# Kernel optimization log

Measured on AMD Instinct MI355X. Metric: run time of the kernel, lower is better.

The kernel has to match this reference:

```python
import jax, jax.numpy as jnp
import numpy as np

TEMPERATURE = 0.5
EPS = 1e-8  # torch CosineSimilarity eps
NEG_INF = -1e9


def setup_inputs() -> dict:
    key = jax.random.key(0)
    k1, k2 = jax.random.split(key)
    B, D = 4096, 256
    return {
        "z_i": jax.random.normal(k1, (B, D), dtype=jnp.float32),
        "z_j": jax.random.normal(k2, (B, D), dtype=jnp.float32),
    }


def reference(z_i, z_j):
    B = z_i.shape[0]
    N = 2 * B
    z = jnp.concatenate([z_i, z_j], axis=0)  # [N, D]
    # Cosine similarity = GEMM of L2-normalized rows (same math as broadcasted CosineSimilarity)
    zn = z / jnp.maximum(jnp.linalg.norm(z, axis=1, keepdims=True), EPS)
    sim = (zn @ zn.T) / TEMPERATURE  # [N, N]
    # Positives: the (i, i+B) and (i+B, i) off-diagonals
    pos = jnp.concatenate([jnp.diagonal(sim, B), jnp.diagonal(sim, -B)])  # [N]
    # CE with label 0 over logits = [positive, negatives...]. The logit set per row
    # equals the sim row minus its self-diagonal entry (positive appears exactly once).
    sim_masked = jnp.where(jnp.eye(N, dtype=bool), NEG_INF, sim)
    lse = jax.nn.logsumexp(sim_masked, axis=1)  # [N]
    # CrossEntropyLoss(reduction='sum') / N == mean over rows
    return jnp.mean(lse - pos)
```

## Files before the change

kernel.cpp:

```cpp
#include <hip/hip_runtime.h>
#include <hip/hip_bf16.h>

#define NN 8192
#define BB 4096
#define DD 256
#define TILE 128
#define NT 64
#define NBLK 2080
#define KSCALE 2.8853900817779268f

typedef __attribute__((ext_vector_type(8))) short short8;
typedef __attribute__((ext_vector_type(4))) float f32x4;

static __device__ __forceinline__ float exp2_fast(float x) {
    float r; asm("v_exp_f32 %0, %1" : "=v"(r) : "v"(x)); return r;
}
static __device__ __forceinline__ ushort f2bf(float x) {
    __hip_bfloat16 h = __float2bfloat16(x);
    return *reinterpret_cast<ushort*>(&h);
}
static __device__ __forceinline__ float bf2f(short u) {
    unsigned int x = (unsigned int)(ushort)u << 16;
    float f; __builtin_memcpy(&f, &x, 4); return f;
}

__global__ __launch_bounds__(256) void norm_kernel(const float* __restrict__ zi,
                                                   const float* __restrict__ zj,
                                                   ushort* __restrict__ zn,
                                                   ushort* __restrict__ zns,
                                                   float* __restrict__ out) {
    if (blockIdx.x == 0 && threadIdx.x == 0) out[0] = 0.f;
    int row  = (blockIdx.x * 256 + threadIdx.x) >> 6;
    int lane = threadIdx.x & 63;
    const float* src = (row < BB) ? (zi + (size_t)row * DD)
                                  : (zj + (size_t)(row - BB) * DD);
    float4 v = ((const float4*)src)[lane];
    float ss = v.x * v.x + v.y * v.y + v.z * v.z + v.w * v.w;
    #pragma unroll
    for (int m = 32; m; m >>= 1) ss += __shfl_xor(ss, m, 64);
    float inv = 1.0f / fmaxf(sqrtf(ss), 1e-8f);
    ushort4 o, os;
    o.x  = f2bf(v.x * inv);            o.y  = f2bf(v.y * inv);
    o.z  = f2bf(v.z * inv);            o.w  = f2bf(v.w * inv);
    float invs = inv * KSCALE;
    os.x = f2bf(v.x * invs);           os.y = f2bf(v.y * invs);
    os.z = f2bf(v.z * invs);           os.w = f2bf(v.w * invs);
    ((ushort4*)(zn  + (size_t)row * DD))[lane] = o;
    ((ushort4*)(zns + (size_t)row * DD))[lane] = os;
}

__global__ __launch_bounds__(256) void sim_kernel(const ushort* __restrict__ zn,
                                                  const ushort* __restrict__ zns,
                                                  float* __restrict__ psum) {
    __shared__ int4  ldsA[2][512];
    __shared__ int4  ldsB[2][512];
    __shared__ float rsumL[2][2][64];
    __shared__ float csumL[2][2][64];

    const int tid  = threadIdx.x;
    const int w    = tid >> 6;
    const int lane = tid & 63;
    const int l15  = lane & 15;
    const int lhi  = lane >> 4;
    const int wr   = w >> 1;
    const int wc   = w & 1;

    int bid = blockIdx.x;
    int idx = (bid & 7) * (NBLK / 8) + (bid >> 3);
    int bj  = (int)((sqrtf(8.0f * (float)idx + 1.0f) - 1.0f) * 0.5f);
    while ((bj + 1) * (bj + 2) / 2 <= idx) ++bj;
    while (bj * (bj + 1) / 2 > idx) --bj;
    int bi = idx - bj * (bj + 1) / 2;

    const int  rowt0   = bi * TILE;
    const int  colt0   = bj * TILE;
    const bool offdiag = (bi != bj);

    auto STAGE = [&](int buf, int k) {
        #pragma unroll
        for (int i = 0; i < 2; ++i) {
            int d = i * 256 + tid;
            int r = d >> 2, g = d & 3;
            const ushort* sa = zns + (size_t)(rowt0 + r) * DD + k * 32 + g * 8;
            __builtin_amdgcn_global_load_lds(
                (__attribute__((address_space(1))) void*)sa,
                (__attribute__((address_space(3))) void*)&ldsA[buf][i * 256 + w * 64],
                16, 0, 0);
            const ushort* sb = zn + (size_t)(colt0 + r) * DD + k * 32 + g * 8;
            __builtin_amdgcn_global_load_lds(
                (__attribute__((address_space(1))) void*)sb,
                (__attribute__((address_space(3))) void*)&ldsB[buf][i * 256 + w * 64],
                16, 0, 0);
        }
    };

    f32x4 acc[4][4];
    #pragma unroll
    for (int mi = 0; mi < 4; ++mi)
        #pragma unroll
        for (int ni = 0; ni < 4; ++ni) acc[mi][ni] = (f32x4){0.f, 0.f, 0.f, 0.f};

    STAGE(0, 0);
    __syncthreads();

    #pragma unroll
    for (int k = 0; k < 8; ++k) {
        if (k < 7) STAGE((k + 1) & 1, k + 1);
        const short8* bufA = (const short8*)ldsA[k & 1];
        const short8* bufB = (const short8*)ldsB[k & 1];
        short8 af[4], bfr[4];
        #pragma unroll
        for (int mi = 0; mi < 4; ++mi)
            af[mi] = bufA[(wr * 64 + mi * 16 + l15) * 4 + lhi];
        #pragma unroll
        for (int ni = 0; ni < 4; ++ni)
            bfr[ni] = bufB[(wc * 64 + ni * 16 + l15) * 4 + lhi];
        #pragma unroll
        for (int mi = 0; mi < 4; ++mi)
            #pragma unroll
            for (int ni = 0; ni < 4; ++ni)
                acc[mi][ni] = __builtin_amdgcn_mfma_f32_16x16x32_bf16(af[mi], bfr[ni], acc[mi][ni], 0, 0, 0);
        __syncthreads();
    }

    float rpart[4][4];
    float cpart[4];
    #pragma unroll
    for (int mi = 0; mi < 4; ++mi)
        #pragma unroll
        for (int g = 0; g < 4; ++g) rpart[mi][g] = 0.f;
    #pragma unroll
    for (int ni = 0; ni < 4; ++ni) cpart[ni] = 0.f;

    #pragma unroll
    for (int mi = 0; mi < 4; ++mi)
        #pragma unroll
        for (int ni = 0; ni < 4; ++ni)
            #pragma unroll
            for (int g = 0; g < 4; ++g) {
                float e = exp2_fast(acc[mi][ni][g]);
                rpart[mi][g] += e;
                cpart[ni]    += e;
            }

    #pragma unroll
    for (int mi = 0; mi < 4; ++mi)
        #pragma unroll
        for (int g = 0; g < 4; ++g) {
            float v = rpart[mi][g];
            v += __shfl_xor(v, 1, 64); v += __shfl_xor(v, 2, 64);
            v += __shfl_xor(v, 4, 64); v += __shfl_xor(v, 8, 64);
            if (l15 == 0) rsumL[wr][wc][mi * 16 + lhi * 4 + g] = v;
        }
    #pragma unroll
    for (int ni = 0; ni < 4; ++ni) {
        float v = cpart[ni];
        v += __shfl_xor(v, 16, 64); v += __shfl_xor(v, 32, 64);
        if (lhi == 0) csumL[wc][wr][ni * 16 + l15] = v;
    }
    __syncthreads();

    if (tid < TILE)
        psum[(size_t)bj * NN + rowt0 + tid] =
            rsumL[tid >> 6][0][tid & 63] + rsumL[tid >> 6][1][tid & 63];
    if (offdiag && tid < TILE)
        psum[(size_t)bi * NN + colt0 + tid] =
            csumL[tid >> 6][0][tid & 63] + csumL[tid >> 6][1][tid & 63];
}

__global__ __launch_bounds__(1024) void reduce_kernel(const ushort* __restrict__ zn,
                                                      const ushort* __restrict__ zns,
                                                      const float* __restrict__ psum,
                                                      float* __restrict__ out) {
    const int tid  = threadIdx.x;
    const int rloc = tid >> 4;
    const int r    = blockIdx.x * 64 + rloc;
    const int l    = tid & 15;

    float S = 0.f;
    #pragma unroll
    for (int i = 0; i < 4; ++i) S += psum[(size_t)(i * 16 + l) * NN + r];

    const ushort* zr = zn  + (size_t)r * DD + l * 16;
    const ushort* sr = zns + (size_t)r * DD + l * 16;
    const ushort* pr = zn  + (size_t)(r ^ BB) * DD + l * 16;
    short8 z0 = *(const short8*)zr, z1 = *(const short8*)(zr + 8);
    short8 s0 = *(const short8*)sr, s1 = *(const short8*)(sr + 8);
    short8 p0 = *(const short8*)pr, p1 = *(const short8*)(pr + 8);
    float ds = 0.f, dp = 0.f;
    #pragma unroll
    for (int k = 0; k < 8; ++k) {
        float za = bf2f(z0[k]), zb = bf2f(z1[k]);
        ds += bf2f(s0[k]) * za + bf2f(s1[k]) * zb;
        dp += bf2f(p0[k]) * za + bf2f(p1[k]) * zb;
    }
    #pragma unroll
    for (int m = 1; m < 16; m <<= 1) {
        S  += __shfl_xor(S,  m, 64);
        ds += __shfl_xor(ds, m, 64);
        dp += __shfl_xor(dp, m, 64);
    }
    __shared__ float red[64];
    if (l == 0) red[rloc] = logf(S - exp2_fast(ds)) - 2.0f * dp;
    __syncthreads();
    if (tid < 64) {
        float v = red[tid];
        #pragma unroll
        for (int m = 32; m; m >>= 1) v += __shfl_xor(v, m, 64);
        if (tid == 0) atomicAdd(out, v * (1.0f / NN));
    }
}

extern "C" void kernel_launch(void* const* d_in, const int* in_sizes, int n_in,
                              void* d_out, int out_size, void* d_ws, size_t ws_size,
                              hipStream_t stream) {
    const float* zi = (const float*)d_in[0];
    const float* zj = (const float*)d_in[1];
    float* out = (float*)d_out;

    char* ws = (char*)d_ws;
    ushort* zn   = (ushort*)ws;
    ushort* zns  = (ushort*)(ws + (size_t)NN * DD * 2);
    float*  psum = (float*)(ws + (size_t)NN * DD * 4);

    norm_kernel<<<NN / 4, 256, 0, stream>>>(zi, zj, zn, zns, out);
    sim_kernel<<<NBLK, 256, 0, stream>>>(zn, zns, psum);
    reduce_kernel<<<NN / 64, 1024, 0, stream>>>(zn, zns, psum, out);
}
```

Baseline: 112.5 us.

## Enlarge sim tiles to 256 with 8 waves, swizzled LDS, and fine-grained waits

```diff
diff --git a/kernel.cpp b/kernel.cpp
--- a/kernel.cpp
+++ b/kernel.cpp
@@ -4,9 +4,10 @@
 #define NN 8192
 #define BB 4096
 #define DD 256
-#define TILE 128
-#define NT 64
-#define NBLK 2080
+#define TILE 256
+#define NT 32
+#define NBLK 528
+#define BK 32
 #define KSCALE 2.8853900817779268f
 
 typedef __attribute__((ext_vector_type(8))) short short8;
@@ -49,21 +50,22 @@
     ((ushort4*)(zns + (size_t)row * DD))[lane] = os;
 }
 
-__global__ __launch_bounds__(256) void sim_kernel(const ushort* __restrict__ zn,
-                                                  const ushort* __restrict__ zns,
-                                                  float* __restrict__ psum) {
-    __shared__ int4  ldsA[2][512];
-    __shared__ int4  ldsB[2][512];
-    __shared__ float rsumL[2][2][64];
-    __shared__ float csumL[2][2][64];
+__global__ __launch_bounds__(512)
+__attribute__((amdgpu_waves_per_eu(2, 2)))
+void sim_kernel(const ushort* __restrict__ zn,
+                const ushort* __restrict__ zns,
+                float* __restrict__ psum) {
+    __shared__ int4  lds4[2][2048];
+    __shared__ float rsum[2][4][128];
+    __shared__ float csum[4][2][64];
 
     const int tid  = threadIdx.x;
     const int w    = tid >> 6;
     const int lane = tid & 63;
     const int l15  = lane & 15;
     const int lhi  = lane >> 4;
-    const int wr   = w >> 1;
-    const int wc   = w & 1;
+    const int wr   = w >> 2;
+    const int wc   = w & 3;
 
     int bid = blockIdx.x;
     int idx = (bid & 7) * (NBLK / 8) + (bid >> 3);
@@ -78,62 +80,70 @@
 
     auto STAGE = [&](int buf, int k) {
         #pragma unroll
-        for (int i = 0; i < 2; ++i) {
-            int d = i * 256 + tid;
-            int r = d >> 2, g = d & 3;
-            const ushort* sa = zns + (size_t)(rowt0 + r) * DD + k * 32 + g * 8;
+        for (int i = 0; i < 4; ++i) {
+            int d = i * 512 + tid;
+            int s = d & 1023;
+            int r = s >> 2, gd = s & 3;
+            int gs = gd ^ ((r >> 2) & 3);
+            const ushort* srcp = (i < 2)
+                ? zns + (size_t)(rowt0 + r) * DD + k * BK + gs * 8
+                : zn  + (size_t)(colt0 + r) * DD + k * BK + gs * 8;
             __builtin_amdgcn_global_load_lds(
-                (__attribute__((address_space(1))) void*)sa,
-                (__attribute__((address_space(3))) void*)&ldsA[buf][i * 256 + w * 64],
+                (__attribute__((address_space(1))) void*)srcp,
+                (__attribute__((address_space(3))) void*)&lds4[buf][i * 512 + w * 64],
                 16, 0, 0);
-            const ushort* sb = zn + (size_t)(colt0 + r) * DD + k * 32 + g * 8;
-            __builtin_amdgcn_global_load_lds(
-                (__attribute__((address_space(1))) void*)sb,
-                (__attribute__((address_space(3))) void*)&ldsB[buf][i * 256 + w * 64],
-                16, 0, 0);
         }
     };
 
-    f32x4 acc[4][4];
-    #pragma unroll
-    for (int mi = 0; mi < 4; ++mi)
+    f32x4 acc[8][4];
+    #pragma unroll
+    for (int mi = 0; mi < 8; ++mi)
         #pragma unroll
         for (int ni = 0; ni < 4; ++ni) acc[mi][ni] = (f32x4){0.f, 0.f, 0.f, 0.f};
 
     STAGE(0, 0);
-    __syncthreads();
+    __builtin_amdgcn_sched_barrier(0);
 
     #pragma unroll
     for (int k = 0; k < 8; ++k) {
         if (k < 7) STAGE((k + 1) & 1, k + 1);
-        const short8* bufA = (const short8*)ldsA[k & 1];
-        const short8* bufB = (const short8*)ldsB[k & 1];
-        short8 af[4], bfr[4];
-        #pragma unroll
-        for (int mi = 0; mi < 4; ++mi)
-            af[mi] = bufA[(wr * 64 + mi * 16 + l15) * 4 + lhi];
-        #pragma unroll
-        for (int ni = 0; ni < 4; ++ni)
-            bfr[ni] = bufB[(wc * 64 + ni * 16 + l15) * 4 + lhi];
-        #pragma unroll
-        for (int mi = 0; mi < 4; ++mi)
+        __builtin_amdgcn_sched_barrier(0);
+        if (k < 7) asm volatile("s_waitcnt vmcnt(4)" ::: "memory");
+        else       asm volatile("s_waitcnt vmcnt(0)" ::: "memory");
+        __builtin_amdgcn_s_barrier();
+        __builtin_amdgcn_sched_barrier(0);
+
+        const short8* bufA = (const short8*)&lds4[k & 1][0];
+        const short8* bufB = (const short8*)&lds4[k & 1][1024];
+        short8 af[8], bf[4];
+        #pragma unroll
+        for (int mi = 0; mi < 8; ++mi) {
+            int r = wr * 128 + mi * 16 + l15;
+            af[mi] = bufA[r * 4 + (lhi ^ ((r >> 2) & 3))];
+        }
+        #pragma unroll
+        for (int ni = 0; ni < 4; ++ni) {
+            int r = wc * 64 + ni * 16 + l15;
+            bf[ni] = bufB[r * 4 + (lhi ^ ((r >> 2) & 3))];
+        }
+        #pragma unroll
+        for (int mi = 0; mi < 8; ++mi)
             #pragma unroll
             for (int ni = 0; ni < 4; ++ni)
-                acc[mi][ni] = __builtin_amdgcn_mfma_f32_16x16x32_bf16(af[mi], bfr[ni], acc[mi][ni], 0, 0, 0);
-        __syncthreads();
-    }
-
-    float rpart[4][4];
+                acc[mi][ni] = __builtin_amdgcn_mfma_f32_16x16x32_bf16(af[mi], bf[ni], acc[mi][ni], 0, 0, 0);
+    }
+
+    float rpart[8][4];
     float cpart[4];
     #pragma unroll
-    for (int mi = 0; mi < 4; ++mi)
+    for (int mi = 0; mi < 8; ++mi)
         #pragma unroll
         for (int g = 0; g < 4; ++g) rpart[mi][g] = 0.f;
     #pragma unroll
     for (int ni = 0; ni < 4; ++ni) cpart[ni] = 0.f;
 
     #pragma unroll
-    for (int mi = 0; mi < 4; ++mi)
+    for (int mi = 0; mi < 8; ++mi)
         #pragma unroll
         for (int ni = 0; ni < 4; ++ni)
             #pragma unroll
@@ -144,28 +154,31 @@
             }
 
     #pragma unroll
-    for (int mi = 0; mi < 4; ++mi)
+    for (int mi = 0; mi < 8; ++mi)
         #pragma unroll
         for (int g = 0; g < 4; ++g) {
             float v = rpart[mi][g];
             v += __shfl_xor(v, 1, 64); v += __shfl_xor(v, 2, 64);
             v += __shfl_xor(v, 4, 64); v += __shfl_xor(v, 8, 64);
-            if (l15 == 0) rsumL[wr][wc][mi * 16 + lhi * 4 + g] = v;
+            if (l15 == 0) rsum[wr][wc][mi * 16 + lhi * 4 + g] = v;
         }
     #pragma unroll
     for (int ni = 0; ni < 4; ++ni) {
         float v = cpart[ni];
         v += __shfl_xor(v, 16, 64); v += __shfl_xor(v, 32, 64);
-        if (lhi == 0) csumL[wc][wr][ni * 16 + l15] = v;
+        if (lhi == 0) csum[wc][wr][ni * 16 + l15] = v;
     }
     __syncthreads();
 
-    if (tid < TILE)
+    if (tid < TILE) {
+        int wrT = tid >> 7, rloc = tid & 127;
         psum[(size_t)bj * NN + rowt0 + tid] =
-            rsumL[tid >> 6][0][tid & 63] + rsumL[tid >> 6][1][tid & 63];
-    if (offdiag && tid < TILE)
-        psum[(size_t)bi * NN + colt0 + tid] =
-            csumL[tid >> 6][0][tid & 63] + csumL[tid >> 6][1][tid & 63];
+            rsum[wrT][0][rloc] + rsum[wrT][1][rloc] + rsum[wrT][2][rloc] + rsum[wrT][3][rloc];
+        if (offdiag) {
+            int wcT = tid >> 6, cloc = tid & 63;
+            psum[(size_t)bi * NN + colt0 + tid] = csum[wcT][0][cloc] + csum[wcT][1][cloc];
+        }
+    }
 }
 
 __global__ __launch_bounds__(1024) void reduce_kernel(const ushort* __restrict__ zn,
@@ -177,9 +190,7 @@
     const int r    = blockIdx.x * 64 + rloc;
     const int l    = tid & 15;
 
-    float S = 0.f;
-    #pragma unroll
-    for (int i = 0; i < 4; ++i) S += psum[(size_t)(i * 16 + l) * NN + r];
+    float S = psum[(size_t)l * NN + r] + psum[(size_t)(16 + l) * NN + r];
 
     const ushort* zr = zn  + (size_t)r * DD + l * 16;
     const ushort* sr = zns + (size_t)r * DD + l * 16;
@@ -224,6 +235,6 @@
     float*  psum = (float*)(ws + (size_t)NN * DD * 4);
 
     norm_kernel<<<NN / 4, 256, 0, stream>>>(zi, zj, zn, zns, out);
-    sim_kernel<<<NBLK, 256, 0, stream>>>(zn, zns, psum);
+    sim_kernel<<<NBLK, 512, 0, stream>>>(zn, zns, psum);
     reduce_kernel<<<NN / 64, 1024, 0, stream>>>(zn, zns, psum, out);
 }
```

New measurement: 107.1 us. 1.05x faster.
